# Kernel tuning notes

Measured on AMD Instinct MI355X. Metric: run time of the kernel, lower is better.

Reference implementation:

```python
import jax, jax.numpy as jnp
import numpy as np
import math

N_EMBD = 1024
NUM_HEADS = 16
MAX_LEN = 2048
AUX = 256
B, T = 2, 2048


def setup_inputs() -> dict:
    key = jax.random.key(0)
    ks = jax.random.split(key, 16)
    s = 0.02
    C, A = N_EMBD, AUX
    inp = {
        "x": jax.random.normal(ks[0], (B, T, C), jnp.float32),
        "aux_x": jax.random.normal(ks[1], (B, T, A), jnp.float32),
        "Wq": s * jax.random.normal(ks[2], (C, C), jnp.float32),
        "bq": jnp.zeros((C,), jnp.float32),
        "Wk": s * jax.random.normal(ks[3], (C + A, C), jnp.float32),
        "bk": jnp.zeros((C,), jnp.float32),
        "Wv": s * jax.random.normal(ks[4], (C + A, C), jnp.float32),
        "bv": jnp.zeros((C,), jnp.float32),
        "Wo": s * jax.random.normal(ks[5], (C, C), jnp.float32),  # zero-init in source; randomized for a meaningful baseline
        "bo": jnp.zeros((C,), jnp.float32),
        "PEq": s * jax.random.normal(ks[6], (MAX_LEN, C), jnp.float32),
        "PEk": s * jax.random.normal(ks[7], (MAX_LEN, C), jnp.float32),
        "attn_mask": jax.random.bernoulli(ks[8], 0.9, (B, T, T)),
        "frame_indices": jax.random.randint(ks[9], (B, T), 0, MAX_LEN),
        "num_heads": NUM_HEADS,
    }
    return inp


def reference(x, aux_x, Wq, bq, Wk, bk, Wv, bv, Wo, bo, PEq, PEk, attn_mask, frame_indices, num_heads):
    Bx, Tx, C = x.shape
    H = num_heads
    hd = C // H
    x_aug = jnp.concatenate([x, aux_x], axis=2)  # [B,T,C+A]
    # QKV projections, split heads; PE added per (position, head) to q and k
    q = (x @ Wq + bq).reshape(Bx, Tx, H, hd) + PEq[frame_indices].reshape(Bx, Tx, H, hd)
    k = (x_aug @ Wk + bk).reshape(Bx, Tx, H, hd) + PEk[frame_indices].reshape(Bx, Tx, H, hd)
    v = (x_aug @ Wv + bv).reshape(Bx, Tx, H, hd)
    scale = 1.0 / math.sqrt(hd)
    scores = jnp.einsum("bqhd,bkhd->bhqk", q, k) * scale  # [B,H,T,T]
    scores = jnp.where(attn_mask[:, None, :, :], scores, -jnp.inf)
    attn = jax.nn.softmax(scores, axis=-1)  # fully-masked rows -> NaN
    out = jnp.einsum("bhqk,bkhd->bqhd", attn, v).reshape(Bx, Tx, C)
    out = jnp.nan_to_num(out, nan=0.0)
    return out @ Wo + bo
```

## Files before the change

### kernel.cpp

```cpp
#include <hip/hip_runtime.h>
#include <hip/hip_bf16.h>

typedef unsigned short u16;
typedef unsigned int u32;
typedef __attribute__((ext_vector_type(8))) short bf16x8;
typedef __attribute__((ext_vector_type(4))) float f32x4;

#define HD 64
#define NH 16
#define TT 2048
#define BB 2
#define CA 1280

__device__ __forceinline__ u16 bfu(float f) {
    u32 u = __builtin_bit_cast(u32, f);
    u32 r = u + 0x7fffu + ((u >> 16) & 1u);
    return (u16)(r >> 16);
}

__device__ __forceinline__ float ex2(float x) {
#if __has_builtin(__builtin_amdgcn_exp2f)
    return __builtin_amdgcn_exp2f(x);
#else
    return exp2f(x);
#endif
}

__device__ __forceinline__ void gload16(const void* g, void* l) {
    __builtin_amdgcn_global_load_lds(
        (const __attribute__((address_space(1))) unsigned int*)g,
        (__attribute__((address_space(3))) unsigned int*)l,
        16, 0, 0);
}

__global__ void prep(const float* __restrict__ x, const float* __restrict__ aux,
                     u16* __restrict__ xa,
                     const float* __restrict__ Wq, const float* __restrict__ Wk,
                     const float* __restrict__ Wv, const float* __restrict__ Wo,
                     u16* __restrict__ WTall, u16* __restrict__ WTo,
                     const unsigned char* __restrict__ m, u32* __restrict__ bits) {
    int bid = blockIdx.x;
    if (bid < 5120) {
        int i = bid * 256 + threadIdx.x;
        int row = i / 320;
        int c4 = i - row * 320;
        float4 v;
        if (c4 < 256) v = ((const float4*)x)[row * 256 + c4];
        else          v = ((const float4*)aux)[row * 64 + (c4 - 256)];
        ushort4 pk; pk.x = bfu(v.x); pk.y = bfu(v.y); pk.z = bfu(v.z); pk.w = bfu(v.w);
        ((ushort4*)xa)[i] = pk;
    } else if (bid < 10240) {
        int t = bid - 5120;
        int z = t / 1280;
        int inner = t - z * 1280;
        int kt = (inner % 40) * 32;
        int nt = (inner / 40) * 32;
        const float* src = (z == 0) ? Wq : (z == 1) ? Wk : (z == 2) ? Wv : Wo;
        u16* dst = (z == 3) ? WTo : WTall + (size_t)z * 1024 * 1280;
        int Ksrc = (z == 0 || z == 3) ? 1024 : 1280;
        int Kpad = (z == 3) ? 1024 : 1280;
        if (kt >= Kpad) return;
        __shared__ float tile[32][33];
        int r = threadIdx.x >> 5, c = threadIdx.x & 31;
        #pragma unroll
        for (int i = 0; i < 4; i++) {
            int k = kt + r + i * 8;
            tile[r + i * 8][c] = (k < Ksrc) ? src[(size_t)k * 1024 + nt + c] : 0.f;
        }
        __syncthreads();
        #pragma unroll
        for (int i = 0; i < 4; i++) {
            int n = nt + r + i * 8;
            dst[(size_t)n * Kpad + kt + c] = bfu(tile[c][r + i * 8]);
        }
    } else {
        __shared__ u32 modeSh;
        if (threadIdx.x == 0) modeSh = 0;
        __syncthreads();
        const u32* wp = (const u32*)m;
        u32 local = 0;
        for (int j = threadIdx.x; j < 2048; j += 256) {
            u32 v = wp[j];
            if (v == 0x3f800000u) local |= 2u;
            else if (v > 1u) local |= 1u;
            if ((j & 1) && v != 0u) local |= 4u;
        }
        if (local) atomicOr(&modeSh, local);
        __syncthreads();
        u32 mode = modeSh;
        bool words32 = (mode & 2u) || (mode == 4u);
        bool bytes8 = !words32 && (mode & 1u);

        int i = (bid - 10240) * 256 + threadIdx.x;
        size_t e0 = (size_t)i * 32;
        u32 r = 0;
        if (words32) {
            const uint4* q = (const uint4*)(wp + e0);
            #pragma unroll
            for (int j4 = 0; j4 < 8; j4++) {
                uint4 v = q[j4];
                if (v.x) r |= 1u << (j4 * 4 + 0);
                if (v.y) r |= 1u << (j4 * 4 + 1);
                if (v.z) r |= 1u << (j4 * 4 + 2);
                if (v.w) r |= 1u << (j4 * 4 + 3);
            }
        } else if (bytes8) {
            const unsigned char* p = m + e0;
            uint4 a = *(const uint4*)p;
            uint4 b = *(const uint4*)(p + 16);
            u32 words[8] = {a.x, a.y, a.z, a.w, b.x, b.y, b.z, b.w};
            #pragma unroll
            for (int jw = 0; jw < 8; jw++) {
                u32 xw = words[jw];
                r |= ((xw >> 0) & 1u) << (jw * 4 + 0);
                r |= ((xw >> 8) & 1u) << (jw * 4 + 1);
                r |= ((xw >> 16) & 1u) << (jw * 4 + 2);
                r |= ((xw >> 24) & 1u) << (jw * 4 + 3);
            }
        } else {
            #pragma unroll 4
            for (int j = 0; j < 32; j++)
                if (wp[(e0 + j) * 2]) r |= 1u << j;
        }
        bits[i] = r;
    }
}

template <int MODE>
__global__ __launch_bounds__(256, 3) void gemm_bt(
    const u16* __restrict__ A, const u16* __restrict__ Bt, int K,
    const float* __restrict__ biasq, const float* __restrict__ biask,
    const float* __restrict__ biasv, const float* __restrict__ PEq,
    const float* __restrict__ PEk, const int* __restrict__ fidx,
    u16* __restrict__ qo, u16* __restrict__ ko, u16* __restrict__ vto,
    float* __restrict__ fo, const float* __restrict__ bo) {
    __shared__ u16 As[128 * 64];
    __shared__ u16 Bs[128 * 64];
    const int tid = threadIdx.x, lane = tid & 63, w = tid >> 6;
    const int l15 = lane & 15, l4 = lane >> 4;
    const int wm = w >> 1, wn = w & 1;
    const int bm = blockIdx.x, bn = blockIdx.y;
    const int Keff = (MODE == 0 && (bn >> 3) == 0) ? 1024 : K;

    f32x4 acc[4][4] = {};

    const int srow = lane >> 3;
    const int schunk = (lane & 7) ^ srow;
    const u16* ag = A + (size_t)(bm * 128 + w * 32 + srow) * K + schunk * 8;
    const u16* bg = Bt + (size_t)(bn * 128 + w * 32 + srow) * K + schunk * 8;
    u16* asl = &As[(w * 32) * 64] + lane * 8;
    u16* bsl = &Bs[(w * 32) * 64] + lane * 8;

    for (int kt = 0; kt < Keff; kt += 64) {
        #pragma unroll
        for (int i = 0; i < 4; i++) {
            gload16(ag + (size_t)i * 8 * K + kt, asl + i * 8 * 64);
            gload16(bg + (size_t)i * 8 * K + kt, bsl + i * 8 * 64);
        }
        __syncthreads();
        #pragma unroll
        for (int ks = 0; ks < 2; ks++) {
            bf16x8 af[4], bfr[4];
            #pragma unroll
            for (int mi = 0; mi < 4; mi++) {
                int row = wm * 64 + mi * 16 + l15;
                af[mi] = *(const bf16x8*)&As[row * 64 + (((ks * 4 + l4) ^ (row & 7)) * 8)];
            }
            #pragma unroll
            for (int ni = 0; ni < 4; ni++) {
                int row = wn * 64 + ni * 16 + l15;
                bfr[ni] = *(const bf16x8*)&Bs[row * 64 + (((ks * 4 + l4) ^ (row & 7)) * 8)];
            }
            #pragma unroll
            for (int mi = 0; mi < 4; mi++)
                #pragma unroll
                for (int ni = 0; ni < 4; ni++)
                    acc[mi][ni] = __builtin_amdgcn_mfma_f32_16x16x32_bf16(
                        af[mi], bfr[ni], acc[mi][ni], 0, 0, 0);
        }
        __syncthreads();
    }

    if (MODE == 0) {
        int sec = bn >> 3;
        if (sec < 2) {
            const float* bias = sec ? biask : biasq;
            const float* PE   = sec ? PEk : PEq;
            u16* outp = sec ? ko : qo;
            float scl = sec ? 1.0f : 0.180336880111120419f;
            #pragma unroll
            for (int mi = 0; mi < 4; mi++) {
                #pragma unroll
                for (int r = 0; r < 4; r++) {
                    int m = bm * 128 + wm * 64 + mi * 16 + l4 * 4 + r;
                    int b = m >> 11, t = m & 2047;
                    int fi = fidx[m];
                    #pragma unroll
                    for (int ni = 0; ni < 4; ni++) {
                        int nn = (bn & 7) * 128 + wn * 64 + ni * 16 + l15;
                        float val = (acc[mi][ni][r] + bias[nn] + PE[(size_t)fi * 1024 + nn]) * scl;
                        outp[((size_t)(b * NH + (nn >> 6)) * TT + t) * HD + (nn & 63)] = bfu(val);
                    }
                }
            }
        } else {
            int b = bm >> 4;
            int t0 = (bm & 15) * 128 + wm * 64;
            #pragma unroll
            for (int ni = 0; ni < 4; ni++) {
                int nn = (bn - 16) * 128 + wn * 64 + ni * 16 + l15;
                float bvv = biasv[nn];
                int h = nn >> 6, d = nn & 63;
                u16* dst = vto + ((size_t)((b * NH + h) * HD + d)) * TT + t0;
                #pragma unroll
                for (int mi = 0; mi < 4; mi++) {
                    ushort4 pk;
                    pk.x = bfu(acc[mi][ni][0] + bvv);
                    pk.y = bfu(acc[mi][ni][1] + bvv);
                    pk.z = bfu(acc[mi][ni][2] + bvv);
                    pk.w = bfu(acc[mi][ni][3] + bvv);
                    *(ushort4*)(dst + mi * 16 + l4 * 4) = pk;
                }
            }
        }
    } else {
        #pragma unroll
        for (int mi = 0; mi < 4; mi++) {
            #pragma unroll
            for (int r = 0; r < 4; r++) {
                int m = bm * 128 + wm * 64 + mi * 16 + l4 * 4 + r;
                #pragma unroll
                for (int ni = 0; ni < 4; ni++) {
                    int ng = bn * 128 + wn * 64 + ni * 16 + l15;
                    fo[(size_t)m * 1024 + ng] = acc[mi][ni][r] + bo[ng];
                }
            }
        }
    }
}

__global__ __launch_bounds__(256, 4) void attn_fwd(
    const u16* __restrict__ Q, const u16* __restrict__ Kg,
    const u16* __restrict__ VT, const u32* __restrict__ mbits,
    u16* __restrict__ Og) {
    __shared__ u16 KPs[64 * 136];
    __shared__ u16 Vs[64 * 128];
    const int tid = threadIdx.x, lane = tid & 63, w = tid >> 6;
    const int l15 = lane & 15, l4 = lane >> 4;
    const int s_ = blockIdx.x;
    const int qt = (s_ >> 3) & 31;
    const int bh = (s_ & 7) * 4 + (s_ >> 8);
    const int b = bh >> 4;
    const size_t hoff = (size_t)bh * (TT * HD);

    bf16x8 qf[2];
    {
        int qbase = qt * 64 + w * 16;
        #pragma unroll
        for (int ks = 0; ks < 2; ks++)
            qf[ks] = *(const bf16x8*)&Q[hoff + (size_t)(qbase + l15) * HD + ks * 32 + l4 * 8];
    }

    bf16x8 ones;
    #pragma unroll
    for (int j = 0; j < 8; j++) ones[j] = (short)0x3F80;

    f32x4 po[4] = {};
    f32x4 pol = {};

    const int srow = lane >> 3;
    const int schunk = (lane & 7) ^ srow;
    const u16* kgl = Kg + hoff + (size_t)(w * 32 + srow) * HD + schunk * 8;
    u16* ksl = &KPs[(w * 32) * 64] + lane * 8;
    const size_t voff = (size_t)bh * (HD * TT);
    const size_t mbase = ((size_t)(b * TT + qt * 64 + w * 16 + l4 * 4)) * 64;
    const int shEven = 31 - l15, shOdd = 15 - l15;

    for (int kt = 0; kt < 16; kt++) {
        uint4 mb[4];
        #pragma unroll
        for (int r = 0; r < 4; r++)
            mb[r] = *(const uint4*)&mbits[mbase + (size_t)r * 64 + kt * 4];

        #pragma unroll
        for (int i = 0; i < 4; i++)
            gload16(kgl + (size_t)(kt * 128 + i * 8) * HD, ksl + i * 8 * 64);
        #pragma unroll
        for (int i = 0; i < 4; i++) {
            int d = w * 16 + i * 4 + l4;
            const u16* src = VT + voff + (size_t)d * TT + kt * 128 + ((l15 ^ (d & 15)) * 8);
            gload16(src, &Vs[(w * 16 + i * 4) * 128] + lane * 8);
        }
        __syncthreads();

        f32x4 s[8];
        __builtin_amdgcn_s_setprio(1);
        #pragma unroll
        for (int nt = 0; nt < 8; nt++) {
            int krow = nt * 16 + l15;
            bf16x8 kf0 = *(const bf16x8*)&KPs[krow * 64 + (((0 + l4) ^ (krow & 7)) * 8)];
            bf16x8 kf1 = *(const bf16x8*)&KPs[krow * 64 + (((4 + l4) ^ (krow & 7)) * 8)];
            f32x4 z = {0.f, 0.f, 0.f, 0.f};
            z = __builtin_amdgcn_mfma_f32_16x16x32_bf16(qf[0], kf0, z, 0, 0, 0);
            s[nt] = __builtin_amdgcn_mfma_f32_16x16x32_bf16(qf[1], kf1, z, 0, 0, 0);
        }
        __builtin_amdgcn_s_setprio(0);
        __syncthreads();

        #pragma unroll
        for (int r = 0; r < 4; r++) {
            u32 mw[4] = {mb[r].x, mb[r].y, mb[r].z, mb[r].w};
            int prow = w * 16 + l4 * 4 + r;
            u16* pw = &KPs[prow * 136 + l15];
            #pragma unroll
            for (int nt = 0; nt < 8; nt++) {
                u32 word = mw[nt >> 1];
                int sh = (nt & 1) ? shOdd : shEven;
                u32 ext = (u32)(((int)(word << sh)) >> 31);
                float p = ex2(s[nt][r]);
                u32 pb = __builtin_bit_cast(u32, p) & ext;
                pw[nt * 16] = (u16)(pb >> 16);
            }
        }

        bf16x8 pf[4];
        #pragma unroll
        for (int ks = 0; ks < 4; ks++)
            pf[ks] = *(const bf16x8*)&KPs[(w * 16 + l15) * 136 + ks * 32 + l4 * 8];
        __builtin_amdgcn_s_setprio(1);
        #pragma unroll
        for (int nto = 0; nto < 4; nto++) {
            #pragma unroll
            for (int ks = 0; ks < 4; ks++) {
                int d = nto * 16 + l15;
                bf16x8 vf = *(const bf16x8*)&Vs[d * 128 + (((ks * 4 + l4) ^ (d & 15)) * 8)];
                po[nto] = __builtin_amdgcn_mfma_f32_16x16x32_bf16(
                    pf[ks], vf, po[nto], 0, 0, 0);
            }
        }
        #pragma unroll
        for (int ks = 0; ks < 4; ks++)
            pol = __builtin_amdgcn_mfma_f32_16x16x32_bf16(pf[ks], ones, pol, 0, 0, 0);
        __builtin_amdgcn_s_setprio(0);
        __syncthreads();
    }

    int h = bh & 15;
    #pragma unroll
    for (int r = 0; r < 4; r++) {
        float lv = pol[r];
        float inv = (lv > 0.f) ? (1.f / lv) : 0.f;
        int t = qt * 64 + w * 16 + l4 * 4 + r;
        #pragma unroll
        for (int nto = 0; nto < 4; nto++)
            Og[((size_t)(b * TT + t)) * 1024 + h * 64 + nto * 16 + l15] =
                bfu(po[nto][r] * inv);
    }
}

extern "C" void kernel_launch(void* const* d_in, const int* in_sizes, int n_in,
                              void* d_out, int out_size, void* d_ws, size_t ws_size,
                              hipStream_t stream) {
    const float* x   = (const float*)d_in[0];
    const float* aux = (const float*)d_in[1];
    const float* Wq  = (const float*)d_in[2];
    const float* bq  = (const float*)d_in[3];
    const float* Wk  = (const float*)d_in[4];
    const float* bk  = (const float*)d_in[5];
    const float* Wv  = (const float*)d_in[6];
    const float* bv  = (const float*)d_in[7];
    const float* Wo  = (const float*)d_in[8];
    const float* bo  = (const float*)d_in[9];
    const float* PEq = (const float*)d_in[10];
    const float* PEk = (const float*)d_in[11];
    const unsigned char* mask = (const unsigned char*)d_in[12];
    const int* fidx  = (const int*)d_in[13];
    float* out = (float*)d_out;

    char* ws = (char*)d_ws;
    u16* XA    = (u16*)(ws + 0);
    u16* AttO  = (u16*)(ws + 0);
    u16* WTall = (u16*)(ws + 10485760);
    u16* WTo   = (u16*)(ws + 18350080);
    u16* Qb    = (u16*)(ws + 20447232);
    u16* Kb    = (u16*)(ws + 28835840);
    u16* VTb   = (u16*)(ws + 45613056);
    u32* MB    = (u32*)(ws + 54001664);

    prep<<<11264, 256, 0, stream>>>(x, aux, XA, Wq, Wk, Wv, Wo, WTall, WTo, mask, MB);

    gemm_bt<0><<<dim3(32, 24), 256, 0, stream>>>(
        XA, WTall, 1280, bq, bk, bv, PEq, PEk, fidx, Qb, Kb, VTb, nullptr, nullptr);

    attn_fwd<<<1024, 256, 0, stream>>>(Qb, Kb, VTb, MB, AttO);

    gemm_bt<1><<<dim3(32, 8), 256, 0, stream>>>(
        AttO, WTo, 1024, nullptr, nullptr, nullptr, nullptr, nullptr, nullptr,
        nullptr, nullptr, nullptr, out, bo);
}
```

Measured before the change: 147.3 us.

## Double attention query tile per block and remap QKV GEMM block order

Each attention block now handles 128 query rows (32 per wave, two MFMA row groups) instead of 64, so every K/V tile staged in shared memory is reused across twice as many queries and the grid halves to 512 blocks. The shared P buffer grows to 128 rows and launch bounds drop to 2 blocks per SM, trading occupancy for reuse and higher register use. The QKV GEMM switches to a 1D grid with a remapped block index that groups M tiles so co-resident blocks share weight columns in cache.

After: 142.1 us. -3.6%, faster.

```diff
diff --git a/kernel.cpp b/kernel.cpp
--- a/kernel.cpp
+++ b/kernel.cpp
@@ -139,7 +139,14 @@
     const int tid = threadIdx.x, lane = tid & 63, w = tid >> 6;
     const int l15 = lane & 15, l4 = lane >> 4;
     const int wm = w >> 1, wn = w & 1;
-    const int bm = blockIdx.x, bn = blockIdx.y;
+    int bm, bn;
+    if (MODE == 0) {
+        int bid = blockIdx.x;
+        bm = (bid & 7) * 4 + ((bid >> 3) & 3);
+        bn = bid >> 5;
+    } else {
+        bm = blockIdx.x; bn = blockIdx.y;
+    }
     const int Keff = (MODE == 0 && (bn >> 3) == 0) ? 1024 : K;
 
     f32x4 acc[4][4] = {};
@@ -239,48 +246,50 @@
     }
 }
 
-__global__ __launch_bounds__(256, 4) void attn_fwd(
+__global__ __launch_bounds__(256, 2) void attn_fwd(
     const u16* __restrict__ Q, const u16* __restrict__ Kg,
     const u16* __restrict__ VT, const u32* __restrict__ mbits,
     u16* __restrict__ Og) {
-    __shared__ u16 KPs[64 * 136];
+    __shared__ u16 KPs[128 * 136];
     __shared__ u16 Vs[64 * 128];
     const int tid = threadIdx.x, lane = tid & 63, w = tid >> 6;
     const int l15 = lane & 15, l4 = lane >> 4;
     const int s_ = blockIdx.x;
-    const int qt = (s_ >> 3) & 31;
-    const int bh = (s_ & 7) * 4 + (s_ >> 8);
+    const int qt = (s_ >> 3) & 15;
+    const int bh = (s_ & 7) * 4 + (s_ >> 7);
     const int b = bh >> 4;
     const size_t hoff = (size_t)bh * (TT * HD);
 
-    bf16x8 qf[2];
-    {
-        int qbase = qt * 64 + w * 16;
+    bf16x8 qf[2][2];
+    #pragma unroll
+    for (int mi = 0; mi < 2; mi++)
         #pragma unroll
         for (int ks = 0; ks < 2; ks++)
-            qf[ks] = *(const bf16x8*)&Q[hoff + (size_t)(qbase + l15) * HD + ks * 32 + l4 * 8];
-    }
+            qf[mi][ks] = *(const bf16x8*)&Q[hoff +
+                (size_t)(qt * 128 + w * 32 + mi * 16 + l15) * HD + ks * 32 + l4 * 8];
 
     bf16x8 ones;
     #pragma unroll
     for (int j = 0; j < 8; j++) ones[j] = (short)0x3F80;
 
-    f32x4 po[4] = {};
-    f32x4 pol = {};
+    f32x4 po[2][4] = {};
+    f32x4 pol[2] = {};
 
     const int srow = lane >> 3;
     const int schunk = (lane & 7) ^ srow;
     const u16* kgl = Kg + hoff + (size_t)(w * 32 + srow) * HD + schunk * 8;
     u16* ksl = &KPs[(w * 32) * 64] + lane * 8;
     const size_t voff = (size_t)bh * (HD * TT);
-    const size_t mbase = ((size_t)(b * TT + qt * 64 + w * 16 + l4 * 4)) * 64;
+    const size_t mbase = ((size_t)(b * TT + qt * 128 + w * 32 + l4 * 4)) * 64;
     const int shEven = 31 - l15, shOdd = 15 - l15;
 
     for (int kt = 0; kt < 16; kt++) {
-        uint4 mb[4];
-        #pragma unroll
-        for (int r = 0; r < 4; r++)
-            mb[r] = *(const uint4*)&mbits[mbase + (size_t)r * 64 + kt * 4];
+        uint4 mb[2][4];
+        #pragma unroll
+        for (int mi = 0; mi < 2; mi++)
+            #pragma unroll
+            for (int r = 0; r < 4; r++)
+                mb[mi][r] = *(const uint4*)&mbits[mbase + (size_t)(mi * 16 + r) * 64 + kt * 4];
 
         #pragma unroll
         for (int i = 0; i < 4; i++)
@@ -293,40 +302,48 @@
         }
         __syncthreads();
 
-        f32x4 s[8];
+        f32x4 s[2][8];
         __builtin_amdgcn_s_setprio(1);
         #pragma unroll
         for (int nt = 0; nt < 8; nt++) {
             int krow = nt * 16 + l15;
             bf16x8 kf0 = *(const bf16x8*)&KPs[krow * 64 + (((0 + l4) ^ (krow & 7)) * 8)];
             bf16x8 kf1 = *(const bf16x8*)&KPs[krow * 64 + (((4 + l4) ^ (krow & 7)) * 8)];
-            f32x4 z = {0.f, 0.f, 0.f, 0.f};
-            z = __builtin_amdgcn_mfma_f32_16x16x32_bf16(qf[0], kf0, z, 0, 0, 0);
-            s[nt] = __builtin_amdgcn_mfma_f32_16x16x32_bf16(qf[1], kf1, z, 0, 0, 0);
+            #pragma unroll
+            for (int mi = 0; mi < 2; mi++) {
+                f32x4 z = {0.f, 0.f, 0.f, 0.f};
+                z = __builtin_amdgcn_mfma_f32_16x16x32_bf16(qf[mi][0], kf0, z, 0, 0, 0);
+                s[mi][nt] = __builtin_amdgcn_mfma_f32_16x16x32_bf16(qf[mi][1], kf1, z, 0, 0, 0);
+            }
         }
         __builtin_amdgcn_s_setprio(0);
         __syncthreads();
 
         #pragma unroll
-        for (int r = 0; r < 4; r++) {
-            u32 mw[4] = {mb[r].x, mb[r].y, mb[r].z, mb[r].w};
-            int prow = w * 16 + l4 * 4 + r;
-            u16* pw = &KPs[prow * 136 + l15];
-            #pragma unroll
-            for (int nt = 0; nt < 8; nt++) {
-                u32 word = mw[nt >> 1];
-                int sh = (nt & 1) ? shOdd : shEven;
-                u32 ext = (u32)(((int)(word << sh)) >> 31);
-                float p = ex2(s[nt][r]);
-                u32 pb = __builtin_bit_cast(u32, p) & ext;
-                pw[nt * 16] = (u16)(pb >> 16);
-            }
-        }
-
-        bf16x8 pf[4];
-        #pragma unroll
-        for (int ks = 0; ks < 4; ks++)
-            pf[ks] = *(const bf16x8*)&KPs[(w * 16 + l15) * 136 + ks * 32 + l4 * 8];
+        for (int mi = 0; mi < 2; mi++) {
+            #pragma unroll
+            for (int r = 0; r < 4; r++) {
+                u32 mw[4] = {mb[mi][r].x, mb[mi][r].y, mb[mi][r].z, mb[mi][r].w};
+                int prow = w * 32 + mi * 16 + l4 * 4 + r;
+                u16* pw = &KPs[prow * 136 + l15];
+                #pragma unroll
+                for (int nt = 0; nt < 8; nt++) {
+                    u32 word = mw[nt >> 1];
+                    int sh = (nt & 1) ? shOdd : shEven;
+                    u32 ext = (u32)(((int)(word << sh)) >> 31);
+                    float p = ex2(s[mi][nt][r]);
+                    u32 pb = __builtin_bit_cast(u32, p) & ext;
+                    pw[nt * 16] = (u16)(pb >> 16);
+                }
+            }
+        }
+
+        bf16x8 pf[2][4];
+        #pragma unroll
+        for (int mi = 0; mi < 2; mi++)
+            #pragma unroll
+            for (int ks = 0; ks < 4; ks++)
+                pf[mi][ks] = *(const bf16x8*)&KPs[(w * 32 + mi * 16 + l15) * 136 + ks * 32 + l4 * 8];
         __builtin_amdgcn_s_setprio(1);
         #pragma unroll
         for (int nto = 0; nto < 4; nto++) {
@@ -334,27 +351,34 @@
             for (int ks = 0; ks < 4; ks++) {
                 int d = nto * 16 + l15;
                 bf16x8 vf = *(const bf16x8*)&Vs[d * 128 + (((ks * 4 + l4) ^ (d & 15)) * 8)];
-                po[nto] = __builtin_amdgcn_mfma_f32_16x16x32_bf16(
-                    pf[ks], vf, po[nto], 0, 0, 0);
-            }
-        }
-        #pragma unroll
-        for (int ks = 0; ks < 4; ks++)
-            pol = __builtin_amdgcn_mfma_f32_16x16x32_bf16(pf[ks], ones, pol, 0, 0, 0);
+                #pragma unroll
+                for (int mi = 0; mi < 2; mi++)
+                    po[mi][nto] = __builtin_amdgcn_mfma_f32_16x16x32_bf16(
+                        pf[mi][ks], vf, po[mi][nto], 0, 0, 0);
+            }
+        }
+        #pragma unroll
+        for (int mi = 0; mi < 2; mi++)
+            #pragma unroll
+            for (int ks = 0; ks < 4; ks++)
+                pol[mi] = __builtin_amdgcn_mfma_f32_16x16x32_bf16(pf[mi][ks], ones, pol[mi], 0, 0, 0);
         __builtin_amdgcn_s_setprio(0);
         __syncthreads();
     }
 
     int h = bh & 15;
     #pragma unroll
-    for (int r = 0; r < 4; r++) {
-        float lv = pol[r];
-        float inv = (lv > 0.f) ? (1.f / lv) : 0.f;
-        int t = qt * 64 + w * 16 + l4 * 4 + r;
-        #pragma unroll
-        for (int nto = 0; nto < 4; nto++)
-            Og[((size_t)(b * TT + t)) * 1024 + h * 64 + nto * 16 + l15] =
-                bfu(po[nto][r] * inv);
+    for (int mi = 0; mi < 2; mi++) {
+        #pragma unroll
+        for (int r = 0; r < 4; r++) {
+            float lv = pol[mi][r];
+            float inv = (lv > 0.f) ? (1.f / lv) : 0.f;
+            int t = qt * 128 + w * 32 + mi * 16 + l4 * 4 + r;
+            #pragma unroll
+            for (int nto = 0; nto < 4; nto++)
+                Og[((size_t)(b * TT + t)) * 1024 + h * 64 + nto * 16 + l15] =
+                    bfu(po[mi][nto][r] * inv);
+        }
     }
 }
 
@@ -389,10 +413,10 @@
 
     prep<<<11264, 256, 0, stream>>>(x, aux, XA, Wq, Wk, Wv, Wo, WTall, WTo, mask, MB);
 
-    gemm_bt<0><<<dim3(32, 24), 256, 0, stream>>>(
+    gemm_bt<0><<<768, 256, 0, stream>>>(
         XA, WTall, 1280, bq, bk, bv, PEq, PEk, fidx, Qb, Kb, VTb, nullptr, nullptr);
 
-    attn_fwd<<<1024, 256, 0, stream>>>(Qb, Kb, VTb, MB, AttO);
+    attn_fwd<<<512, 256, 0, stream>>>(Qb, Kb, VTb, MB, AttO);
 
     gemm_bt<1><<<dim3(32, 8), 256, 0, stream>>>(
         AttO, WTo, 1024, nullptr, nullptr, nullptr, nullptr, nullptr, nullptr,
```
